# Kernel optimization log

Measured on AMD Instinct MI355X. Metric: run time of the kernel, lower is better.

Reference implementation:

```python
import jax, jax.numpy as jnp
import numpy as np

B, T, N, K1, H, C = 2, 8, 5000, 17, 4, 16  # K1 = self + 16 neighbors
N_OUT = (C + 1) // 2


def setup_inputs() -> dict:
    key = jax.random.key(0)
    kf, kn, km = jax.random.split(key, 3)
    # small scale so exp(-||Mdf||^2) stays in a numerically interesting range
    features = jax.random.normal(kf, (B, T, N, H, C), dtype=jnp.float32) * 0.1
    nearest = jax.random.randint(kn, (N, K1), 0, N, dtype=jnp.int32)
    nearest = nearest.at[:, 0].set(jnp.arange(N, dtype=jnp.int32))  # col 0 = self
    drop = (jax.random.uniform(km, (N, K1)) < 0.05) & (jnp.arange(K1)[None, :] > 0)
    nearest = jnp.where(drop, jnp.int32(-1), nearest)
    # faithful parameter init: [I | 0] blocks scaled by Q1_init / Q2_init, diag(M_init)
    q_form = jnp.zeros((H, N_OUT, C), dtype=jnp.float32).at[:, :, :N_OUT].set(jnp.eye(N_OUT, dtype=jnp.float32))
    multiQ1 = q_form * 1.2
    multiQ2 = q_form * 0.8
    multiM = jnp.broadcast_to(jnp.eye(C, dtype=jnp.float32), (H, C, C)) * 1.5
    return {"features": features, "nearest_nodes": nearest,
            "multiQ1": multiQ1, "multiQ2": multiQ2, "multiM": multiM}


def reference(features, nearest_nodes, multiQ1, multiQ2, multiM):
    B_, T_, N_, H_, C_ = features.shape
    # pad row N_ is all-zeros; -1 sentinel indices are routed to it
    pad = jnp.concatenate([features, jnp.zeros_like(features[:, :, :1])], axis=2)  # (B,T,N+1,H,C)
    idx = jnp.where(nearest_nodes < 0, N_, nearest_nodes)  # (N, K1)

    # ---------------- undirected ----------------
    nbr = idx[:, 1:]                       # (N, K) neighbor indices (excl. self)
    fj = pad[:, :, nbr]                    # (B,T,N,K,H,C) gathered neighbor feats
    df = features[:, :, :, None] - fj      # (B,T,N,K,H,C)
    Mdf = jnp.einsum('hij,btnkhj->btnkhi', multiM, df)
    w = jnp.exp(-jnp.sum(Mdf * Mdf, axis=-1))              # (B,T,N,K,H)
    valid = (nearest_nodes[:, 1:] >= 0)[None, None, :, :, None]
    w = w * valid
    deg = jnp.sum(w, axis=3)                               # (B,T,N,H)
    pad_deg = jnp.concatenate([deg, jnp.zeros_like(deg[:, :, :1])], axis=2)
    deg_j = pad_deg[:, :, nbr]                             # (B,T,N,K,H)
    dmul = jnp.sqrt(deg[:, :, :, None] * deg_j)
    inv = jnp.where(dmul > 0, 1.0 / jnp.where(dmul > 0, dmul, 1.0), 0.0)
    u_w = w * inv                                          # (B,T,N,K,H)

    # ---------------- directed ----------------
    fi = pad[:, :-1, idx]                                  # (B,T-1,N,K1,H,C)
    Qi = jnp.einsum('hij,btnkhj->btnkhi', multiQ1, fi)     # (B,T-1,N,K1,H,n_out)
    Qj = jnp.einsum('hij,btnhj->btnhi', multiQ2, features[:, 1:])  # (B,T-1,N,H,n_out)
    wd = jnp.exp(-jnp.sum(Qi * Qj[:, :, :, None], axis=-1))        # (B,T-1,N,K1,H)
    wd = wd * (nearest_nodes >= 0)[None, None, :, :, None]
    in_deg = jnp.sum(wd, axis=3)                           # (B,T-1,N,H)
    inv_d = jnp.where(in_deg > 0, 1.0 / jnp.where(in_deg > 0, in_deg, 1.0), 0.0)
    d_w = wd * inv_d[:, :, :, None]                        # (B,T-1,N,K1,H)

    return (u_w, d_w)
```

## Files before the change

kernel.cpp:

```cpp
#include <hip/hip_runtime.h>
#include <cstdio>

#define BB 2
#define TT 8
#define NNODE 5000
#define KK1 17
#define HH 4
#define NT (BB*TT*NNODE)
#define NE2 (BB*7*NNODE*HH)

typedef unsigned short u16;
typedef unsigned int u32;

__device__ __forceinline__ u16 f2bf(float x) {
  u32 u = __float_as_uint(x);
  u32 r = (u + 0x7fffu + ((u >> 16) & 1u)) >> 16;
  return (u16)r;
}
__device__ __forceinline__ float bfLo(u32 w){ return __uint_as_float(w << 16); }
__device__ __forceinline__ float bfHi(u32 w){ return __uint_as_float(w & 0xffff0000u); }

__global__ void __launch_bounds__(256) k_prep(
    const float* __restrict__ feat, const float* __restrict__ mm,
    const float* __restrict__ q1, const float* __restrict__ q2,
    u16* __restrict__ g, u16* __restrict__ a8, u16* __restrict__ b8) {
  const int lane = threadIdx.x & 63;
  const int h = lane >> 4, i = lane & 15;
  const int bid = blockIdx.x;
  const int x = bid & 7;
  const int local = (bid >> 3) * 4 + (threadIdx.x >> 6);
  const int mbase = x * 10000 + local * 10;
  float Mrow[16], Qrow[16];
  const float* qsrc = (i < 8) ? (q1 + (h*8 + i)*16) : (q2 + (h*8 + (i - 8))*16);
#pragma unroll
  for (int j = 0; j < 16; ++j) {
    Mrow[j] = mm[(h*16 + i)*16 + j];
    Qrow[j] = qsrc[j];
  }
  for (int l = 0; l < 10; ++l) {
    const int m = mbase + l;
    const float4* fp = reinterpret_cast<const float4*>(feat + (size_t)m*64 + h*16);
    float fv[16];
#pragma unroll
    for (int q = 0; q < 4; ++q) {
      float4 v = fp[q];
      fv[q*4+0] = v.x; fv[q*4+1] = v.y; fv[q*4+2] = v.z; fv[q*4+3] = v.w;
    }
    float accG = 0.f, accQ = 0.f;
#pragma unroll
    for (int j = 0; j < 16; ++j) {
      accG = fmaf(Mrow[j], fv[j], accG);
      accQ = fmaf(Qrow[j], fv[j], accQ);
    }
    g[(size_t)m*64 + lane] = f2bf(accG);
    if (i < 8) a8[(size_t)m*32 + h*8 + i] = f2bf(accQ);
    else       b8[(size_t)m*32 + h*8 + (i - 8)] = f2bf(accQ);
  }
}

__global__ void __launch_bounds__(256) k_deg(
    const u16* __restrict__ g, const int* __restrict__ nn,
    float* __restrict__ deg, u16* __restrict__ wbuf) {
  const int bid = blockIdx.x;
  const int work = ((bid & 7) * 2500) + (bid >> 3);
  const int m = work*4 + (threadIdx.x >> 6);
  const int lane = threadIdx.x & 63;
  const int k = lane >> 2, h = lane & 3;
  const int n = m % NNODE;
  const int btbase = m - n;
  int jr = nn[n*KK1 + 1 + k];
  bool valid = jr >= 0;
  int j = valid ? jr : 0;
  const uint4* pi = reinterpret_cast<const uint4*>(g + (size_t)m*64 + h*16);
  const uint4* pj = reinterpret_cast<const uint4*>(g + (size_t)(btbase + j)*64 + h*16);
  uint4 A0 = pi[0], A1 = pi[1];
  uint4 B0 = pj[0], B1 = pj[1];
  u32 aw[8] = {A0.x,A0.y,A0.z,A0.w,A1.x,A1.y,A1.z,A1.w};
  u32 bw[8] = {B0.x,B0.y,B0.z,B0.w,B1.x,B1.y,B1.z,B1.w};
  float dot = 0.f, si = 0.f, sj = 0.f;
#pragma unroll
  for (int r = 0; r < 8; ++r) {
    float al = bfLo(aw[r]), ah = bfHi(aw[r]);
    float bl = bfLo(bw[r]), bh = bfHi(bw[r]);
    dot = fmaf(al, bl, dot); dot = fmaf(ah, bh, dot);
    si  = fmaf(al, al, si);  si  = fmaf(ah, ah, si);
    sj  = fmaf(bl, bl, sj);  sj  = fmaf(bh, bh, sj);
  }
  float e = si + sj - 2.f*dot;
  float w = valid ? __expf(-e) : 0.f;
  wbuf[(size_t)m*64 + lane] = f2bf(w);
  float dsum = w;
  dsum += __shfl_xor(dsum, 4);
  dsum += __shfl_xor(dsum, 8);
  dsum += __shfl_xor(dsum, 16);
  dsum += __shfl_xor(dsum, 32);
  if (lane < 4) deg[m*4 + lane] = dsum;
}

__global__ void __launch_bounds__(256) k_uw(
    const u16* __restrict__ wbuf, const int* __restrict__ nn,
    const float* __restrict__ deg, float* __restrict__ uw) {
  const int bid = blockIdx.x;
  const int wg = ((bid & 7) * 625) + (bid >> 3);
  const int idx4 = (wg * 256 + threadIdx.x) * 4;
  const int m = idx4 >> 6;
  const int r = idx4 & 63;
  const int k = r >> 2;
  const int n = m % NNODE;
  const int btbase = m - n;
  uint2 wv = *reinterpret_cast<const uint2*>(wbuf + idx4);
  float w0 = bfLo(wv.x), w1 = bfHi(wv.x), w2 = bfLo(wv.y), w3 = bfHi(wv.y);
  float4 out = {0.f, 0.f, 0.f, 0.f};
  int jr = nn[n*KK1 + 1 + k];
  if (jr >= 0) {
    float4 di = *reinterpret_cast<const float4*>(deg + (size_t)m*4);
    float4 dj = *reinterpret_cast<const float4*>(deg + (size_t)(btbase + jr)*4);
    float m0 = di.x*dj.x, m1 = di.y*dj.y, m2 = di.z*dj.z, m3 = di.w*dj.w;
    out.x = (w0 > 0.f && m0 > 0.f) ? w0 * rsqrtf(m0) : 0.f;
    out.y = (w1 > 0.f && m1 > 0.f) ? w1 * rsqrtf(m1) : 0.f;
    out.z = (w2 > 0.f && m2 > 0.f) ? w2 * rsqrtf(m2) : 0.f;
    out.w = (w3 > 0.f && m3 > 0.f) ? w3 * rsqrtf(m3) : 0.f;
  }
  *reinterpret_cast<float4*>(uw + idx4) = out;
}

__global__ void __launch_bounds__(256) k_dw(
    const u16* __restrict__ a8, const u16* __restrict__ b8,
    const int* __restrict__ nn, float* __restrict__ dw) {
  const int bid = blockIdx.x;
  const int wg = (bid & 7) * 137 + (bid >> 3);
  const int t0 = wg * 256 + threadIdx.x;
  if (t0 >= NE2) return;
  const int h = t0 & 3;
  const int rest = t0 >> 2;
  const int n = rest % NNODE;
  const int q = rest / NNODE;
  const int b = q / 7, t = q % 7;
  uint4 Bv = *reinterpret_cast<const uint4*>(b8 + ((size_t)((b*TT + t + 1)*NNODE + n))*32 + h*8);
  float bv[8] = {bfLo(Bv.x), bfHi(Bv.x), bfLo(Bv.y), bfHi(Bv.y),
                 bfLo(Bv.z), bfHi(Bv.z), bfLo(Bv.w), bfHi(Bv.w)};
  const int nbase = n*KK1;
  const int abase = (b*TT + t)*NNODE;
  float wk[17];
  float indeg = 0.f;
#pragma unroll
  for (int k = 0; k < KK1; ++k) {
    int jr = nn[nbase + k];
    bool valid = jr >= 0;
    int j = valid ? jr : 0;
    uint4 Av = *reinterpret_cast<const uint4*>(a8 + ((size_t)(abase + j))*32 + h*8);
    float dot = 0.f;
    dot = fmaf(bfLo(Av.x), bv[0], dot); dot = fmaf(bfHi(Av.x), bv[1], dot);
    dot = fmaf(bfLo(Av.y), bv[2], dot); dot = fmaf(bfHi(Av.y), bv[3], dot);
    dot = fmaf(bfLo(Av.z), bv[4], dot); dot = fmaf(bfHi(Av.z), bv[5], dot);
    dot = fmaf(bfLo(Av.w), bv[6], dot); dot = fmaf(bfHi(Av.w), bv[7], dot);
    float w = valid ? __expf(-dot) : 0.f;
    wk[k] = w;
    indeg += w;
  }
  float inv = (indeg > 0.f) ? (1.0f / indeg) : 0.f;
  float* o = dw + ((size_t)(b*7 + t)*NNODE + n)*68;
#pragma unroll
  for (int k = 0; k < KK1; ++k) o[k*4 + h] = wk[k] * inv;
}

extern "C" void kernel_launch(void* const* d_in, const int* in_sizes, int n_in,
                              void* d_out, int out_size, void* d_ws, size_t ws_size,
                              hipStream_t stream) {
  const float* feat = (const float*)d_in[0];
  const int*   nn   = (const int*)d_in[1];
  const float* q1   = (const float*)d_in[2];
  const float* q2   = (const float*)d_in[3];
  const float* mm   = (const float*)d_in[4];
  float* uw = (float*)d_out;
  float* dw = uw + (size_t)NT*64;
  u16*   wstage = (u16*)dw;

  const size_t G_BYTES  = (size_t)NT*64*2;
  const size_t A_BYTES  = (size_t)NT*32*2;
  const size_t DEG_BYTES= (size_t)NT*4*4;
  const size_t NEED = G_BYTES + 2*A_BYTES + DEG_BYTES;
  if (ws_size < NEED) {
    fprintf(stderr, "kernel_launch: ws_size %zu < needed %zu\n", ws_size, NEED);
    return;
  }
  u16*   g   = (u16*)d_ws;
  u16*   a8  = (u16*)((char*)d_ws + G_BYTES);
  u16*   b8  = (u16*)((char*)d_ws + G_BYTES + A_BYTES);
  float* deg = (float*)((char*)d_ws + G_BYTES + 2*A_BYTES);

  k_prep<<<2000, 256, 0, stream>>>(feat, mm, q1, q2, g, a8, b8);
  k_deg <<<20000, 256, 0, stream>>>(g, nn, deg, wstage);
  k_uw  <<<5000, 256, 0, stream>>>(wstage, nn, deg, uw);
  k_dw  <<<1096, 256, 0, stream>>>(a8, b8, nn, dw);
}
```

Measured before the change: 64.06 us.

## Coarsen deg/uw kernels per thread and stage dw output through LDS

k_deg now has each wavefront process two nodes, and k_uw has each thread handle eight outputs (two neighbors) instead of four, which halves the grid sizes and gives each thread more independent memory work. k_dw now computes each 64-row tile into shared memory and writes it out as contiguous float4 chunks, replacing the strided scalar stores. The grid mappings are rebalanced across the 8 XCD groups. Costs are more registers per thread and an added LDS buffer plus barrier in k_dw, which may lower occupancy.

```diff
diff --git a/kernel.cpp b/kernel.cpp
--- a/kernel.cpp
+++ b/kernel.cpp
@@ -7,7 +7,7 @@
 #define KK1 17
 #define HH 4
 #define NT (BB*TT*NNODE)
-#define NE2 (BB*7*NNODE*HH)
+#define NREST (BB*7*NNODE)
 
 typedef unsigned short u16;
 typedef unsigned int u32;
@@ -19,6 +19,21 @@
 }
 __device__ __forceinline__ float bfLo(u32 w){ return __uint_as_float(w << 16); }
 __device__ __forceinline__ float bfHi(u32 w){ return __uint_as_float(w & 0xffff0000u); }
+
+__device__ __forceinline__ float edge_e(uint4 A0, uint4 A1, uint4 B0, uint4 B1) {
+  u32 aw[8] = {A0.x,A0.y,A0.z,A0.w,A1.x,A1.y,A1.z,A1.w};
+  u32 bw[8] = {B0.x,B0.y,B0.z,B0.w,B1.x,B1.y,B1.z,B1.w};
+  float dot = 0.f, si = 0.f, sj = 0.f;
+#pragma unroll
+  for (int r = 0; r < 8; ++r) {
+    float al = bfLo(aw[r]), ah = bfHi(aw[r]);
+    float bl = bfLo(bw[r]), bh = bfHi(bw[r]);
+    dot = fmaf(al, bl, dot); dot = fmaf(ah, bh, dot);
+    si  = fmaf(al, al, si);  si  = fmaf(ah, ah, si);
+    sj  = fmaf(bl, bl, sj);  sj  = fmaf(bh, bh, sj);
+  }
+  return si + sj - 2.f*dot;
+}
 
 __global__ void __launch_bounds__(256) k_prep(
     const float* __restrict__ feat, const float* __restrict__ mm,
@@ -62,106 +77,131 @@
     const u16* __restrict__ g, const int* __restrict__ nn,
     float* __restrict__ deg, u16* __restrict__ wbuf) {
   const int bid = blockIdx.x;
-  const int work = ((bid & 7) * 2500) + (bid >> 3);
-  const int m = work*4 + (threadIdx.x >> 6);
+  const int work = ((bid & 7) * 1250) + (bid >> 3);
+  const int p = work*4 + (threadIdx.x >> 6);
+  const int m0 = p*2, m1 = m0 + 1;
   const int lane = threadIdx.x & 63;
   const int k = lane >> 2, h = lane & 3;
-  const int n = m % NNODE;
-  const int btbase = m - n;
-  int jr = nn[n*KK1 + 1 + k];
-  bool valid = jr >= 0;
-  int j = valid ? jr : 0;
-  const uint4* pi = reinterpret_cast<const uint4*>(g + (size_t)m*64 + h*16);
-  const uint4* pj = reinterpret_cast<const uint4*>(g + (size_t)(btbase + j)*64 + h*16);
-  uint4 A0 = pi[0], A1 = pi[1];
-  uint4 B0 = pj[0], B1 = pj[1];
-  u32 aw[8] = {A0.x,A0.y,A0.z,A0.w,A1.x,A1.y,A1.z,A1.w};
-  u32 bw[8] = {B0.x,B0.y,B0.z,B0.w,B1.x,B1.y,B1.z,B1.w};
-  float dot = 0.f, si = 0.f, sj = 0.f;
-#pragma unroll
-  for (int r = 0; r < 8; ++r) {
-    float al = bfLo(aw[r]), ah = bfHi(aw[r]);
-    float bl = bfLo(bw[r]), bh = bfHi(bw[r]);
-    dot = fmaf(al, bl, dot); dot = fmaf(ah, bh, dot);
-    si  = fmaf(al, al, si);  si  = fmaf(ah, ah, si);
-    sj  = fmaf(bl, bl, sj);  sj  = fmaf(bh, bh, sj);
-  }
-  float e = si + sj - 2.f*dot;
-  float w = valid ? __expf(-e) : 0.f;
-  wbuf[(size_t)m*64 + lane] = f2bf(w);
-  float dsum = w;
-  dsum += __shfl_xor(dsum, 4);
-  dsum += __shfl_xor(dsum, 8);
-  dsum += __shfl_xor(dsum, 16);
-  dsum += __shfl_xor(dsum, 32);
-  if (lane < 4) deg[m*4 + lane] = dsum;
+  const int n0 = m0 % NNODE, n1 = m1 % NNODE;
+  const int bt0 = m0 - n0, bt1 = m1 - n1;
+  int jr0 = nn[n0*KK1 + 1 + k];
+  int jr1 = nn[n1*KK1 + 1 + k];
+  bool v0 = jr0 >= 0, v1 = jr1 >= 0;
+  int j0 = v0 ? jr0 : 0;
+  int j1 = v1 ? jr1 : 0;
+  const uint4* pi0 = reinterpret_cast<const uint4*>(g + (size_t)m0*64 + h*16);
+  const uint4* pi1 = reinterpret_cast<const uint4*>(g + (size_t)m1*64 + h*16);
+  const uint4* pj0 = reinterpret_cast<const uint4*>(g + (size_t)(bt0 + j0)*64 + h*16);
+  const uint4* pj1 = reinterpret_cast<const uint4*>(g + (size_t)(bt1 + j1)*64 + h*16);
+  uint4 A00 = pi0[0], A01 = pi0[1];
+  uint4 A10 = pi1[0], A11 = pi1[1];
+  uint4 B00 = pj0[0], B01 = pj0[1];
+  uint4 B10 = pj1[0], B11 = pj1[1];
+  float e0 = edge_e(A00, A01, B00, B01);
+  float e1 = edge_e(A10, A11, B10, B11);
+  float w0 = v0 ? __expf(-e0) : 0.f;
+  float w1 = v1 ? __expf(-e1) : 0.f;
+  wbuf[(size_t)m0*64 + lane] = f2bf(w0);
+  wbuf[(size_t)m1*64 + lane] = f2bf(w1);
+  float d0 = w0, d1 = w1;
+  d0 += __shfl_xor(d0, 4);  d1 += __shfl_xor(d1, 4);
+  d0 += __shfl_xor(d0, 8);  d1 += __shfl_xor(d1, 8);
+  d0 += __shfl_xor(d0, 16); d1 += __shfl_xor(d1, 16);
+  d0 += __shfl_xor(d0, 32); d1 += __shfl_xor(d1, 32);
+  if (lane < 4) {
+    deg[m0*4 + lane] = d0;
+    deg[m1*4 + lane] = d1;
+  }
 }
 
 __global__ void __launch_bounds__(256) k_uw(
     const u16* __restrict__ wbuf, const int* __restrict__ nn,
     const float* __restrict__ deg, float* __restrict__ uw) {
   const int bid = blockIdx.x;
-  const int wg = ((bid & 7) * 625) + (bid >> 3);
-  const int idx4 = (wg * 256 + threadIdx.x) * 4;
-  const int m = idx4 >> 6;
-  const int r = idx4 & 63;
-  const int k = r >> 2;
+  const int x = bid & 7, sub = bid >> 3;
+  const int wg = (x < 4 ? x*313 : 4*313 + (x-4)*312) + sub;
+  const int idx8 = (wg * 256 + threadIdx.x) * 8;
+  const int m = idx8 >> 6;
+  const int r8 = idx8 & 63;
+  const int k0 = r8 >> 2;
   const int n = m % NNODE;
-  const int btbase = m - n;
-  uint2 wv = *reinterpret_cast<const uint2*>(wbuf + idx4);
-  float w0 = bfLo(wv.x), w1 = bfHi(wv.x), w2 = bfLo(wv.y), w3 = bfHi(wv.y);
-  float4 out = {0.f, 0.f, 0.f, 0.f};
-  int jr = nn[n*KK1 + 1 + k];
-  if (jr >= 0) {
-    float4 di = *reinterpret_cast<const float4*>(deg + (size_t)m*4);
-    float4 dj = *reinterpret_cast<const float4*>(deg + (size_t)(btbase + jr)*4);
-    float m0 = di.x*dj.x, m1 = di.y*dj.y, m2 = di.z*dj.z, m3 = di.w*dj.w;
-    out.x = (w0 > 0.f && m0 > 0.f) ? w0 * rsqrtf(m0) : 0.f;
-    out.y = (w1 > 0.f && m1 > 0.f) ? w1 * rsqrtf(m1) : 0.f;
-    out.z = (w2 > 0.f && m2 > 0.f) ? w2 * rsqrtf(m2) : 0.f;
-    out.w = (w3 > 0.f && m3 > 0.f) ? w3 * rsqrtf(m3) : 0.f;
-  }
-  *reinterpret_cast<float4*>(uw + idx4) = out;
+  const int btb = m - n;
+  uint4 wv = *reinterpret_cast<const uint4*>(wbuf + idx8);
+  int jr0 = nn[n*KK1 + 1 + k0];
+  int jr1 = nn[n*KK1 + 2 + k0];
+  float4 di = *reinterpret_cast<const float4*>(deg + (size_t)m*4);
+  float4 o0 = {0.f,0.f,0.f,0.f}, o1 = {0.f,0.f,0.f,0.f};
+  if (jr0 >= 0) {
+    float4 dj = *reinterpret_cast<const float4*>(deg + (size_t)(btb + jr0)*4);
+    float w0 = bfLo(wv.x), w1 = bfHi(wv.x), w2 = bfLo(wv.y), w3 = bfHi(wv.y);
+    float p0 = di.x*dj.x, p1 = di.y*dj.y, p2 = di.z*dj.z, p3 = di.w*dj.w;
+    o0.x = (w0 > 0.f && p0 > 0.f) ? w0 * rsqrtf(p0) : 0.f;
+    o0.y = (w1 > 0.f && p1 > 0.f) ? w1 * rsqrtf(p1) : 0.f;
+    o0.z = (w2 > 0.f && p2 > 0.f) ? w2 * rsqrtf(p2) : 0.f;
+    o0.w = (w3 > 0.f && p3 > 0.f) ? w3 * rsqrtf(p3) : 0.f;
+  }
+  if (jr1 >= 0) {
+    float4 dj = *reinterpret_cast<const float4*>(deg + (size_t)(btb + jr1)*4);
+    float w0 = bfLo(wv.z), w1 = bfHi(wv.z), w2 = bfLo(wv.w), w3 = bfHi(wv.w);
+    float p0 = di.x*dj.x, p1 = di.y*dj.y, p2 = di.z*dj.z, p3 = di.w*dj.w;
+    o1.x = (w0 > 0.f && p0 > 0.f) ? w0 * rsqrtf(p0) : 0.f;
+    o1.y = (w1 > 0.f && p1 > 0.f) ? w1 * rsqrtf(p1) : 0.f;
+    o1.z = (w2 > 0.f && p2 > 0.f) ? w2 * rsqrtf(p2) : 0.f;
+    o1.w = (w3 > 0.f && p3 > 0.f) ? w3 * rsqrtf(p3) : 0.f;
+  }
+  *reinterpret_cast<float4*>(uw + idx8)     = o0;
+  *reinterpret_cast<float4*>(uw + idx8 + 4) = o1;
 }
 
 __global__ void __launch_bounds__(256) k_dw(
     const u16* __restrict__ a8, const u16* __restrict__ b8,
     const int* __restrict__ nn, float* __restrict__ dw) {
-  const int bid = blockIdx.x;
-  const int wg = (bid & 7) * 137 + (bid >> 3);
-  const int t0 = wg * 256 + threadIdx.x;
-  if (t0 >= NE2) return;
-  const int h = t0 & 3;
-  const int rest = t0 >> 2;
-  const int n = rest % NNODE;
-  const int q = rest / NNODE;
-  const int b = q / 7, t = q % 7;
-  uint4 Bv = *reinterpret_cast<const uint4*>(b8 + ((size_t)((b*TT + t + 1)*NNODE + n))*32 + h*8);
-  float bv[8] = {bfLo(Bv.x), bfHi(Bv.x), bfLo(Bv.y), bfHi(Bv.y),
-                 bfLo(Bv.z), bfHi(Bv.z), bfLo(Bv.w), bfHi(Bv.w)};
-  const int nbase = n*KK1;
-  const int abase = (b*TT + t)*NNODE;
-  float wk[17];
-  float indeg = 0.f;
-#pragma unroll
-  for (int k = 0; k < KK1; ++k) {
-    int jr = nn[nbase + k];
-    bool valid = jr >= 0;
-    int j = valid ? jr : 0;
-    uint4 Av = *reinterpret_cast<const uint4*>(a8 + ((size_t)(abase + j))*32 + h*8);
-    float dot = 0.f;
-    dot = fmaf(bfLo(Av.x), bv[0], dot); dot = fmaf(bfHi(Av.x), bv[1], dot);
-    dot = fmaf(bfLo(Av.y), bv[2], dot); dot = fmaf(bfHi(Av.y), bv[3], dot);
-    dot = fmaf(bfLo(Av.z), bv[4], dot); dot = fmaf(bfHi(Av.z), bv[5], dot);
-    dot = fmaf(bfLo(Av.w), bv[6], dot); dot = fmaf(bfHi(Av.w), bv[7], dot);
-    float w = valid ? __expf(-dot) : 0.f;
-    wk[k] = w;
-    indeg += w;
-  }
-  float inv = (indeg > 0.f) ? (1.0f / indeg) : 0.f;
-  float* o = dw + ((size_t)(b*7 + t)*NNODE + n)*68;
-#pragma unroll
-  for (int k = 0; k < KK1; ++k) o[k*4 + h] = wk[k] * inv;
+  __shared__ float lds[64*68];
+  const int bid = blockIdx.x;
+  const int x = bid & 7, sub = bid >> 3;
+  const int wg = (x < 6 ? x*137 : 6*137 + (x-6)*136) + sub;
+  const int lr = threadIdx.x >> 2;
+  const int h  = threadIdx.x & 3;
+  const int rest = wg*64 + lr;
+  if (rest < NREST) {
+    const int n = rest % NNODE;
+    const int q2 = rest / NNODE;
+    const int b = q2 / 7, t = q2 % 7;
+    uint4 Bv = *reinterpret_cast<const uint4*>(b8 + ((size_t)((b*TT + t + 1)*NNODE + n))*32 + h*8);
+    float bv[8] = {bfLo(Bv.x), bfHi(Bv.x), bfLo(Bv.y), bfHi(Bv.y),
+                   bfLo(Bv.z), bfHi(Bv.z), bfLo(Bv.w), bfHi(Bv.w)};
+    const int nbase = n*KK1;
+    const int abase = (b*TT + t)*NNODE;
+    float wk[17];
+    float indeg = 0.f;
+#pragma unroll
+    for (int kk = 0; kk < KK1; ++kk) {
+      int jr = nn[nbase + kk];
+      bool valid = jr >= 0;
+      int j = valid ? jr : 0;
+      uint4 Av = *reinterpret_cast<const uint4*>(a8 + ((size_t)(abase + j))*32 + h*8);
+      float dot = 0.f;
+      dot = fmaf(bfLo(Av.x), bv[0], dot); dot = fmaf(bfHi(Av.x), bv[1], dot);
+      dot = fmaf(bfLo(Av.y), bv[2], dot); dot = fmaf(bfHi(Av.y), bv[3], dot);
+      dot = fmaf(bfLo(Av.z), bv[4], dot); dot = fmaf(bfHi(Av.z), bv[5], dot);
+      dot = fmaf(bfLo(Av.w), bv[6], dot); dot = fmaf(bfHi(Av.w), bv[7], dot);
+      float w = valid ? __expf(-dot) : 0.f;
+      wk[kk] = w;
+      indeg += w;
+    }
+    float inv = (indeg > 0.f) ? (1.0f / indeg) : 0.f;
+#pragma unroll
+    for (int kk = 0; kk < KK1; ++kk) lds[lr*68 + kk*4 + h] = wk[kk] * inv;
+  }
+  __syncthreads();
+  const int rows = NREST - wg*64;
+  const int nchunks = (rows >= 64 ? 64 : rows) * 17;
+  float4* obase = reinterpret_cast<float4*>(dw + (size_t)wg*4352);
+  for (int c = threadIdx.x; c < nchunks; c += 256) {
+    const int row = c / 17;
+    const int col = (c % 17) * 4;
+    obase[c] = *reinterpret_cast<const float4*>(&lds[row*68 + col]);
+  }
 }
 
 extern "C" void kernel_launch(void* const* d_in, const int* in_sizes, int n_in,
@@ -190,7 +230,7 @@
   float* deg = (float*)((char*)d_ws + G_BYTES + 2*A_BYTES);
 
   k_prep<<<2000, 256, 0, stream>>>(feat, mm, q1, q2, g, a8, b8);
-  k_deg <<<20000, 256, 0, stream>>>(g, nn, deg, wstage);
-  k_uw  <<<5000, 256, 0, stream>>>(wstage, nn, deg, uw);
-  k_dw  <<<1096, 256, 0, stream>>>(a8, b8, nn, dw);
-}
+  k_deg <<<10000, 256, 0, stream>>>(g, nn, deg, wstage);
+  k_uw  <<<2500, 256, 0, stream>>>(wstage, nn, deg, uw);
+  k_dw  <<<1094, 256, 0, stream>>>(a8, b8, nn, dw);
+}
```

New measurement: 61.29 us. 4.3% less time.

## Transpose staging buffers to node-major layout so gathers cover all batch-time slices

Applied to the files above, without the earlier changes.

Precomputed projections are now stored node-major, with all 16 batch-time slices of a node contiguous. A neighbor gather then fetches one contiguous 2KB block instead of 16 scattered rows. Degree, undirected-weight and directed-weight kernels are reorganized to one block (or wave) per node, and outputs are transposed through LDS for coalesced writes. Weights are staged in fp32 in workspace rather than bf16 in the output buffer, which adds extra workspace traffic and LDS barriers.

```diff
diff --git a/kernel.cpp b/kernel.cpp
--- a/kernel.cpp
+++ b/kernel.cpp
@@ -7,7 +7,8 @@
 #define KK1 17
 #define HH 4
 #define NT (BB*TT*NNODE)
-#define NE2 (BB*7*NNODE*HH)
+#define NSLICE 16
+#define NREST (BB*7*NNODE)
 
 typedef unsigned short u16;
 typedef unsigned int u32;
@@ -23,7 +24,7 @@
 __global__ void __launch_bounds__(256) k_prep(
     const float* __restrict__ feat, const float* __restrict__ mm,
     const float* __restrict__ q1, const float* __restrict__ q2,
-    u16* __restrict__ g, u16* __restrict__ a8, u16* __restrict__ b8) {
+    u16* __restrict__ gT, u16* __restrict__ a8T, u16* __restrict__ b8T) {
   const int lane = threadIdx.x & 63;
   const int h = lane >> 4, i = lane & 15;
   const int bid = blockIdx.x;
@@ -37,8 +38,12 @@
     Mrow[j] = mm[(h*16 + i)*16 + j];
     Qrow[j] = qsrc[j];
   }
+#pragma unroll 2
   for (int l = 0; l < 10; ++l) {
     const int m = mbase + l;
+    const int off = local*10 + l;
+    const int bt = 2*x + (off >= NNODE);
+    const int n = m - bt*NNODE;
     const float4* fp = reinterpret_cast<const float4*>(feat + (size_t)m*64 + h*16);
     float fv[16];
 #pragma unroll
@@ -52,116 +57,136 @@
       accG = fmaf(Mrow[j], fv[j], accG);
       accQ = fmaf(Qrow[j], fv[j], accQ);
     }
-    g[(size_t)m*64 + lane] = f2bf(accG);
-    if (i < 8) a8[(size_t)m*32 + h*8 + i] = f2bf(accQ);
-    else       b8[(size_t)m*32 + h*8 + (i - 8)] = f2bf(accQ);
-  }
-}
-
-__global__ void __launch_bounds__(256) k_deg(
-    const u16* __restrict__ g, const int* __restrict__ nn,
-    float* __restrict__ deg, u16* __restrict__ wbuf) {
-  const int bid = blockIdx.x;
-  const int work = ((bid & 7) * 2500) + (bid >> 3);
-  const int m = work*4 + (threadIdx.x >> 6);
-  const int lane = threadIdx.x & 63;
-  const int k = lane >> 2, h = lane & 3;
-  const int n = m % NNODE;
-  const int btbase = m - n;
-  int jr = nn[n*KK1 + 1 + k];
-  bool valid = jr >= 0;
-  int j = valid ? jr : 0;
-  const uint4* pi = reinterpret_cast<const uint4*>(g + (size_t)m*64 + h*16);
-  const uint4* pj = reinterpret_cast<const uint4*>(g + (size_t)(btbase + j)*64 + h*16);
-  uint4 A0 = pi[0], A1 = pi[1];
-  uint4 B0 = pj[0], B1 = pj[1];
+    gT[(size_t)n*1024 + bt*64 + lane] = f2bf(accG);
+    if (i < 8) a8T[(size_t)n*512 + bt*32 + h*8 + i] = f2bf(accQ);
+    else       b8T[(size_t)n*512 + bt*32 + h*8 + (i - 8)] = f2bf(accQ);
+  }
+}
+
+__global__ void __launch_bounds__(256) k_deg2(
+    const u16* __restrict__ gT, const int* __restrict__ nn,
+    float* __restrict__ degT, float* __restrict__ wstage) {
+  __shared__ float red[4][64];
+  const int n = blockIdx.x;
+  const int lane = threadIdx.x & 63;
+  const int kq = __builtin_amdgcn_readfirstlane(threadIdx.x >> 6);
+  const int bt = lane >> 2;
+  const int h  = lane & 3;
+  const uint4* po = reinterpret_cast<const uint4*>(gT + (size_t)n*1024 + bt*64 + h*16);
+  uint4 A0 = po[0], A1 = po[1];
   u32 aw[8] = {A0.x,A0.y,A0.z,A0.w,A1.x,A1.y,A1.z,A1.w};
-  u32 bw[8] = {B0.x,B0.y,B0.z,B0.w,B1.x,B1.y,B1.z,B1.w};
-  float dot = 0.f, si = 0.f, sj = 0.f;
+  float av[16];
+  float si = 0.f;
 #pragma unroll
   for (int r = 0; r < 8; ++r) {
-    float al = bfLo(aw[r]), ah = bfHi(aw[r]);
-    float bl = bfLo(bw[r]), bh = bfHi(bw[r]);
-    dot = fmaf(al, bl, dot); dot = fmaf(ah, bh, dot);
-    si  = fmaf(al, al, si);  si  = fmaf(ah, ah, si);
-    sj  = fmaf(bl, bl, sj);  sj  = fmaf(bh, bh, sj);
-  }
-  float e = si + sj - 2.f*dot;
-  float w = valid ? __expf(-e) : 0.f;
-  wbuf[(size_t)m*64 + lane] = f2bf(w);
-  float dsum = w;
-  dsum += __shfl_xor(dsum, 4);
-  dsum += __shfl_xor(dsum, 8);
-  dsum += __shfl_xor(dsum, 16);
-  dsum += __shfl_xor(dsum, 32);
-  if (lane < 4) deg[m*4 + lane] = dsum;
-}
-
-__global__ void __launch_bounds__(256) k_uw(
-    const u16* __restrict__ wbuf, const int* __restrict__ nn,
-    const float* __restrict__ deg, float* __restrict__ uw) {
-  const int bid = blockIdx.x;
-  const int wg = ((bid & 7) * 625) + (bid >> 3);
-  const int idx4 = (wg * 256 + threadIdx.x) * 4;
-  const int m = idx4 >> 6;
-  const int r = idx4 & 63;
-  const int k = r >> 2;
-  const int n = m % NNODE;
-  const int btbase = m - n;
-  uint2 wv = *reinterpret_cast<const uint2*>(wbuf + idx4);
-  float w0 = bfLo(wv.x), w1 = bfHi(wv.x), w2 = bfLo(wv.y), w3 = bfHi(wv.y);
-  float4 out = {0.f, 0.f, 0.f, 0.f};
-  int jr = nn[n*KK1 + 1 + k];
-  if (jr >= 0) {
-    float4 di = *reinterpret_cast<const float4*>(deg + (size_t)m*4);
-    float4 dj = *reinterpret_cast<const float4*>(deg + (size_t)(btbase + jr)*4);
-    float m0 = di.x*dj.x, m1 = di.y*dj.y, m2 = di.z*dj.z, m3 = di.w*dj.w;
-    out.x = (w0 > 0.f && m0 > 0.f) ? w0 * rsqrtf(m0) : 0.f;
-    out.y = (w1 > 0.f && m1 > 0.f) ? w1 * rsqrtf(m1) : 0.f;
-    out.z = (w2 > 0.f && m2 > 0.f) ? w2 * rsqrtf(m2) : 0.f;
-    out.w = (w3 > 0.f && m3 > 0.f) ? w3 * rsqrtf(m3) : 0.f;
-  }
-  *reinterpret_cast<float4*>(uw + idx4) = out;
-}
-
-__global__ void __launch_bounds__(256) k_dw(
-    const u16* __restrict__ a8, const u16* __restrict__ b8,
+    av[2*r]   = bfLo(aw[r]);
+    av[2*r+1] = bfHi(aw[r]);
+    si = fmaf(av[2*r], av[2*r], si);
+    si = fmaf(av[2*r+1], av[2*r+1], si);
+  }
+  float dsum = 0.f;
+#pragma unroll
+  for (int kk = 0; kk < 4; ++kk) {
+    const int k = kq*4 + kk;
+    int jr = nn[n*KK1 + 1 + k];
+    bool v = jr >= 0;
+    int j = v ? jr : 0;
+    const uint4* pj = reinterpret_cast<const uint4*>(gT + (size_t)j*1024 + bt*64 + h*16);
+    uint4 B0 = pj[0], B1 = pj[1];
+    u32 bw[8] = {B0.x,B0.y,B0.z,B0.w,B1.x,B1.y,B1.z,B1.w};
+    float dot = 0.f, sj = 0.f;
+#pragma unroll
+    for (int r = 0; r < 8; ++r) {
+      float bl = bfLo(bw[r]), bh = bfHi(bw[r]);
+      dot = fmaf(av[2*r], bl, dot); dot = fmaf(av[2*r+1], bh, dot);
+      sj  = fmaf(bl, bl, sj);       sj  = fmaf(bh, bh, sj);
+    }
+    float e = si + sj - 2.f*dot;
+    float w = v ? __expf(-e) : 0.f;
+    wstage[(size_t)n*1024 + k*64 + lane] = w;
+    dsum += w;
+  }
+  red[kq][lane] = dsum;
+  __syncthreads();
+  if (kq == 0) {
+    float d = red[0][lane] + red[1][lane] + red[2][lane] + red[3][lane];
+    degT[(size_t)n*64 + lane] = d;
+  }
+}
+
+__global__ void __launch_bounds__(256) k_uw2(
+    const float* __restrict__ wstage, const int* __restrict__ nn,
+    const float* __restrict__ degT, float* __restrict__ uw) {
+  __shared__ float outl[16*72];
+  const int n = blockIdx.x;
+  const int lane = threadIdx.x & 63;
+  const int kq = __builtin_amdgcn_readfirstlane(threadIdx.x >> 6);
+  float di = degT[(size_t)n*64 + lane];
+#pragma unroll
+  for (int kk = 0; kk < 4; ++kk) {
+    const int k = kq*4 + kk;
+    int jr = nn[n*KK1 + 1 + k];
+    int j = (jr >= 0) ? jr : 0;
+    float dj = degT[(size_t)j*64 + lane];
+    float w  = wstage[(size_t)n*1024 + k*64 + lane];
+    float p = di * dj;
+    outl[k*72 + lane] = (p > 0.f) ? w * rsqrtf(p) : 0.f;
+  }
+  __syncthreads();
+  const int c = threadIdx.x;
+  const int bt = c >> 4, q = c & 15;
+  float4 val = *reinterpret_cast<const float4*>(&outl[q*72 + bt*4]);
+  float4* ob = reinterpret_cast<float4*>(uw);
+  ob[(size_t)bt*80000 + n*16 + q] = val;
+}
+
+__global__ void __launch_bounds__(256) k_dw2(
+    const u16* __restrict__ a8T, const u16* __restrict__ b8T,
     const int* __restrict__ nn, float* __restrict__ dw) {
-  const int bid = blockIdx.x;
-  const int wg = (bid & 7) * 137 + (bid >> 3);
-  const int t0 = wg * 256 + threadIdx.x;
-  if (t0 >= NE2) return;
-  const int h = t0 & 3;
-  const int rest = t0 >> 2;
-  const int n = rest % NNODE;
-  const int q = rest / NNODE;
-  const int b = q / 7, t = q % 7;
-  uint4 Bv = *reinterpret_cast<const uint4*>(b8 + ((size_t)((b*TT + t + 1)*NNODE + n))*32 + h*8);
+  __shared__ float lds[4*14*68];
+  const int wv = __builtin_amdgcn_readfirstlane(threadIdx.x >> 6);
+  const int n = blockIdx.x*4 + wv;
+  const int lane = threadIdx.x & 63;
+  const int btv = lane >> 2;
+  const int h = lane & 3;
+  const bool alive = btv < 14;
+  const int btc = alive ? btv : 0;
+  const int b = btc / 7, t = btc % 7;
+  uint4 Bv = *reinterpret_cast<const uint4*>(b8T + (size_t)n*512 + (b*8 + t + 1)*32 + h*8);
   float bv[8] = {bfLo(Bv.x), bfHi(Bv.x), bfLo(Bv.y), bfHi(Bv.y),
                  bfLo(Bv.z), bfHi(Bv.z), bfLo(Bv.w), bfHi(Bv.w)};
-  const int nbase = n*KK1;
-  const int abase = (b*TT + t)*NNODE;
+  const int bta = b*8 + t;
   float wk[17];
   float indeg = 0.f;
 #pragma unroll
   for (int k = 0; k < KK1; ++k) {
-    int jr = nn[nbase + k];
-    bool valid = jr >= 0;
-    int j = valid ? jr : 0;
-    uint4 Av = *reinterpret_cast<const uint4*>(a8 + ((size_t)(abase + j))*32 + h*8);
+    int jr = nn[n*KK1 + k];
+    bool v = jr >= 0;
+    int j = v ? jr : 0;
+    uint4 Av = *reinterpret_cast<const uint4*>(a8T + (size_t)j*512 + bta*32 + h*8);
     float dot = 0.f;
     dot = fmaf(bfLo(Av.x), bv[0], dot); dot = fmaf(bfHi(Av.x), bv[1], dot);
     dot = fmaf(bfLo(Av.y), bv[2], dot); dot = fmaf(bfHi(Av.y), bv[3], dot);
     dot = fmaf(bfLo(Av.z), bv[4], dot); dot = fmaf(bfHi(Av.z), bv[5], dot);
     dot = fmaf(bfLo(Av.w), bv[6], dot); dot = fmaf(bfHi(Av.w), bv[7], dot);
-    float w = valid ? __expf(-dot) : 0.f;
+    float w = v ? __expf(-dot) : 0.f;
     wk[k] = w;
     indeg += w;
   }
   float inv = (indeg > 0.f) ? (1.0f / indeg) : 0.f;
-  float* o = dw + ((size_t)(b*7 + t)*NNODE + n)*68;
-#pragma unroll
-  for (int k = 0; k < KK1; ++k) o[k*4 + h] = wk[k] * inv;
+  if (alive) {
+#pragma unroll
+    for (int k = 0; k < KK1; ++k) lds[(wv*14 + btv)*68 + k*4 + h] = wk[k] * inv;
+  }
+  __syncthreads();
+  const int n0 = blockIdx.x*4;
+  for (int c = threadIdx.x; c < 4*14*17; c += 256) {
+    const int row = c / 17;
+    const int col = (c % 17) * 4;
+    const int wvv = row / 14, btr = row % 14;
+    float4 val = *reinterpret_cast<const float4*>(&lds[row*68 + col]);
+    *reinterpret_cast<float4*>(dw + ((size_t)btr*NNODE + n0 + wvv)*68 + col) = val;
+  }
 }
 
 extern "C" void kernel_launch(void* const* d_in, const int* in_sizes, int n_in,
@@ -174,23 +199,24 @@
   const float* mm   = (const float*)d_in[4];
   float* uw = (float*)d_out;
   float* dw = uw + (size_t)NT*64;
-  u16*   wstage = (u16*)dw;
-
-  const size_t G_BYTES  = (size_t)NT*64*2;
-  const size_t A_BYTES  = (size_t)NT*32*2;
-  const size_t DEG_BYTES= (size_t)NT*4*4;
-  const size_t NEED = G_BYTES + 2*A_BYTES + DEG_BYTES;
+
+  const size_t GT_BYTES = (size_t)NNODE*1024*2;
+  const size_t AT_BYTES = (size_t)NNODE*512*2;
+  const size_t DG_BYTES = (size_t)NNODE*64*4;
+  const size_t WS_BYTES = (size_t)NNODE*1024*4;
+  const size_t NEED = GT_BYTES + 2*AT_BYTES + DG_BYTES + WS_BYTES;
   if (ws_size < NEED) {
     fprintf(stderr, "kernel_launch: ws_size %zu < needed %zu\n", ws_size, NEED);
     return;
   }
-  u16*   g   = (u16*)d_ws;
-  u16*   a8  = (u16*)((char*)d_ws + G_BYTES);
-  u16*   b8  = (u16*)((char*)d_ws + G_BYTES + A_BYTES);
-  float* deg = (float*)((char*)d_ws + G_BYTES + 2*A_BYTES);
-
-  k_prep<<<2000, 256, 0, stream>>>(feat, mm, q1, q2, g, a8, b8);
-  k_deg <<<20000, 256, 0, stream>>>(g, nn, deg, wstage);
-  k_uw  <<<5000, 256, 0, stream>>>(wstage, nn, deg, uw);
-  k_dw  <<<1096, 256, 0, stream>>>(a8, b8, nn, dw);
-}
+  u16*   gT   = (u16*)d_ws;
+  u16*   a8T  = (u16*)((char*)d_ws + GT_BYTES);
+  u16*   b8T  = (u16*)((char*)d_ws + GT_BYTES + AT_BYTES);
+  float* degT = (float*)((char*)d_ws + GT_BYTES + 2*AT_BYTES);
+  float* wst  = (float*)((char*)d_ws + GT_BYTES + 2*AT_BYTES + DG_BYTES);
+
+  k_prep<<<2000, 256, 0, stream>>>(feat, mm, q1, q2, gT, a8T, b8T);
+  k_deg2<<<NNODE, 256, 0, stream>>>(gT, nn, degT, wst);
+  k_uw2 <<<NNODE, 256, 0, stream>>>(wst, nn, degT, uw);
+  k_dw2 <<<NNODE/4, 256, 0, stream>>>(a8T, b8T, nn, dw);
+}
```

Result: slower. 69.38 us (+8.3%).
